# Kernel optimization log

Hardware: AMD Instinct MI355X
Metric: run time of the kernel (lower is better)

The kernel has to match this reference:

```python
import jax, jax.numpy as jnp
import numpy as np

N_NODES = 100000
N_EDGES = 3200000


def setup_inputs() -> dict:
    key = jax.random.key(0)
    ks = jax.random.split(key, 8)
    n_in, h1, h2 = 512, 512, 128
    # xavier-uniform-ish scaling for weights
    lim1 = (6.0 / (n_in + h1)) ** 0.5
    lim2 = (6.0 / (h1 + h2)) ** 0.5
    return {
        "seq_a": jax.random.normal(ks[0], (N_NODES, n_in), dtype=jnp.float32),
        "W1": jax.random.uniform(ks[1], (n_in, h1), jnp.float32, -lim1, lim1),
        "b1": jnp.zeros((h1,), jnp.float32),
        "W2": jax.random.uniform(ks[2], (h1, h2), jnp.float32, -lim2, lim2),
        "b2": jnp.zeros((h2,), jnp.float32),
        "adj_rows": jnp.sort(jax.random.randint(ks[3], (N_EDGES,), 0, N_NODES, jnp.int32)),
        "adj_cols": jax.random.randint(ks[4], (N_EDGES,), 0, N_NODES, jnp.int32),
        "adj_vals": jax.random.uniform(ks[5], (N_EDGES,), jnp.float32),
    }


def reference(seq_a, W1, b1, W2, b2, adj_rows, adj_cols, adj_vals):
    # Eval-mode forward: F.dropout is identity when training=False.
    # MLP: Linear(n_in,512) + ReLU, Linear(512,128) (no activation on last layer)
    h = jax.nn.relu(seq_a @ W1 + b1)          # [N, 512]
    h_a = h @ W2 + b2                          # [N, 128]
    # Sparse aggregation: h_p = adj @ h_a with adj in COO form.
    # h_p[r] = sum over edges e with row r of vals[e] * h_a[cols[e]]
    msgs = adj_vals[:, None] * h_a[adj_cols]   # [E, 128] irregular gather
    h_p = jax.ops.segment_sum(msgs, adj_rows, num_segments=N_NODES)  # [N, 128]
    return (h_a, h_p)
```

## Files before the change

kernel.cpp:

```cpp
#include <hip/hip_runtime.h>

#define N_NODES 100000
#define ROWS_PAD 100096
#define NIN 512
#define H1  512
#define H2  128
#define N_EDGES 3200000

typedef __attribute__((ext_vector_type(8))) short bf16x8;
typedef __attribute__((ext_vector_type(4))) float f32x4;
typedef __attribute__((ext_vector_type(2))) float f32x2;

__device__ __forceinline__ unsigned short f2b(float x) {
  union { float f; unsigned int u; } c; c.f = x;
  unsigned int u = c.u;
  unsigned int r = (u + 0x7FFFu + ((u >> 16) & 1u)) >> 16;
  return (unsigned short)r;
}

typedef const __attribute__((address_space(1))) unsigned int* gp1_t;
typedef __attribute__((address_space(3))) unsigned int* sp3_t;
__device__ __forceinline__ void gl_lds16(const void* g, void* s) {
  __builtin_amdgcn_global_load_lds((gp1_t)g, (sp3_t)s, 16, 0, 0);
}

__global__ void prep_a_kernel(const float* __restrict__ A, unsigned short* __restrict__ A1) {
  int idx = blockIdx.x * blockDim.x + threadIdx.x;
  int stride = gridDim.x * blockDim.x;
  for (int i = idx; i < N_NODES * 64; i += stride) {
    int n = i >> 6;
    int kb = (i & 63) << 3;
    int ks = kb ^ ((n & 7) << 3);
    const float* src = A + ((size_t)n << 9) + ks;
    float4 v0 = *(const float4*)src;
    float4 v1 = *(const float4*)(src + 4);
    uint4 p;
    p.x = (unsigned)f2b(v0.x) | ((unsigned)f2b(v0.y) << 16);
    p.y = (unsigned)f2b(v0.z) | ((unsigned)f2b(v0.w) << 16);
    p.z = (unsigned)f2b(v1.x) | ((unsigned)f2b(v1.y) << 16);
    p.w = (unsigned)f2b(v1.z) | ((unsigned)f2b(v1.w) << 16);
    *(uint4*)(A1 + ((size_t)n << 9) + kb) = p;
  }
}

__global__ void prep_w_kernel(const float* __restrict__ W1, const float* __restrict__ W2,
                              unsigned short* __restrict__ W1t, unsigned short* __restrict__ W2t) {
  int idx = blockIdx.x * blockDim.x + threadIdx.x;
  int stride = gridDim.x * blockDim.x;
  for (int i = idx; i < H1 * NIN; i += stride) {
    int n = i >> 9, k = i & 511;
    W1t[i] = f2b(W1[(size_t)(k ^ ((n & 7) << 3)) * H1 + n]);
  }
  for (int i = idx; i < H2 * H1; i += stride) {
    int n = i >> 9, k = i & 511;
    W2t[i] = f2b(W2[(size_t)(k ^ ((n & 7) << 3)) * H2 + n]);
  }
}

__global__ void rowptr_kernel(const int* __restrict__ rows, int* __restrict__ row_ptr) {
  int idx = blockIdx.x * blockDim.x + threadIdx.x;
  int stride = gridDim.x * blockDim.x;
  for (int e = idx; e < N_EDGES; e += stride) {
    int r = rows[e];
    int rp = (e == 0) ? -1 : rows[e - 1];
    for (int q = rp + 1; q <= r; ++q) row_ptr[q] = e;
  }
  int lastrow = rows[N_EDGES - 1];
  for (int q = idx; q <= N_NODES; q += stride)
    if (q > lastrow) row_ptr[q] = N_EDGES;
}

__global__ __launch_bounds__(256, 5) void gemm1_kernel(
    const unsigned short* __restrict__ A1, const unsigned short* __restrict__ W1t,
    const float* __restrict__ b1, unsigned short* __restrict__ h_pre)
{
  __shared__ __align__(16) unsigned short SM[12288];
  const int tid = threadIdx.x;
  const int w = tid >> 6, lane = tid & 63;
  const int l15 = lane & 15, lg = lane >> 4;
  const int wr = w & 1, wc = w >> 1;
  const int hw = blockIdx.x;
  const int work = (hw & 7) * 782 + (hw >> 3);
  const int row0 = (work >> 2) << 6;
  const int n0 = (work & 3) << 7;

  f32x4 acc[2][4];
  #pragma unroll
  for (int m = 0; m < 2; ++m)
    #pragma unroll
    for (int n = 0; n < 4; ++n) acc[m][n] = (f32x4){0.f, 0.f, 0.f, 0.f};

  const int so = tid * 16;
  for (int kt = 0; kt < 8; ++kt) {
    #pragma unroll
    for (int it = 0; it < 2; ++it) {
      int o = it * 4096 + so;
      int r = o >> 7, kb = o & 127;
      gl_lds16((const char*)A1 + (((size_t)(row0 + r)) << 10) + (kt << 7) + kb, (char*)SM + o);
    }
    #pragma unroll
    for (int it = 0; it < 4; ++it) {
      int o = it * 4096 + so;
      int r = o >> 7, kb = o & 127;
      gl_lds16((const char*)W1t + (((size_t)(n0 + r)) << 10) + (kt << 7) + kb, (char*)SM + 8192 + o);
    }
    __syncthreads();
    #pragma unroll
    for (int ks = 0; ks < 2; ++ks) {
      bf16x8 af[2], bfr[4];
      #pragma unroll
      for (int m = 0; m < 2; ++m) {
        int r = wr * 32 + m * 16 + l15;
        af[m] = *(const bf16x8*)((const char*)SM + (r << 7) + (((ks << 6) + (lg << 4)) ^ ((r & 7) << 4)));
      }
      #pragma unroll
      for (int n = 0; n < 4; ++n) {
        int r = wc * 64 + n * 16 + l15;
        bfr[n] = *(const bf16x8*)((const char*)SM + 8192 + (r << 7) + (((ks << 6) + (lg << 4)) ^ ((r & 7) << 4)));
      }
      #pragma unroll
      for (int m = 0; m < 2; ++m)
        #pragma unroll
        for (int n = 0; n < 4; ++n)
          acc[m][n] = __builtin_amdgcn_mfma_f32_16x16x32_bf16(af[m], bfr[n], acc[m][n], 0, 0, 0);
    }
    __syncthreads();
  }

  #pragma unroll
  for (int n = 0; n < 4; ++n) {
    int cl = wc * 64 + n * 16 + l15;
    float bias = b1[n0 + cl];
    #pragma unroll
    for (int m = 0; m < 2; ++m) {
      #pragma unroll
      for (int q = 0; q < 4; ++q) {
        int rl = wr * 32 + m * 16 + lg * 4 + q;
        float v = acc[m][n][q] + bias;
        v = v > 0.f ? v : 0.f;
        SM[rl * 128 + (cl ^ ((rl & 7) << 3))] = f2b(v);
      }
    }
  }
  __syncthreads();
  #pragma unroll
  for (int p = 0; p < 4; ++p) {
    int ch = tid + p * 256;
    int row = ch >> 4, six = ch & 15;
    uint4 d = *(const uint4*)((const char*)SM + (ch << 4));
    *(uint4*)((char*)h_pre + (((size_t)(row0 + row)) << 10) + (n0 << 1) + (six << 4)) = d;
  }
}

__global__ __launch_bounds__(256, 5) void gemm2_kernel(
    const unsigned short* __restrict__ Hp, const unsigned short* __restrict__ W2t,
    const float* __restrict__ b2, float* __restrict__ ha_out, unsigned char* __restrict__ ha8)
{
  __shared__ __align__(16) unsigned short SM[12288];
  const int tid = threadIdx.x;
  const int w = tid >> 6, lane = tid & 63;
  const int l15 = lane & 15, lg = lane >> 4;
  const int wr = w & 1, wc = w >> 1;
  const int row0 = blockIdx.x << 6;

  f32x4 acc[2][4];
  #pragma unroll
  for (int m = 0; m < 2; ++m)
    #pragma unroll
    for (int n = 0; n < 4; ++n) acc[m][n] = (f32x4){0.f, 0.f, 0.f, 0.f};

  const int so = tid * 16;
  for (int kt = 0; kt < 8; ++kt) {
    #pragma unroll
    for (int it = 0; it < 2; ++it) {
      int o = it * 4096 + so;
      int r = o >> 7, kb = o & 127;
      gl_lds16((const char*)Hp + (((size_t)(row0 + r)) << 10) + (kt << 7) + kb, (char*)SM + o);
    }
    #pragma unroll
    for (int it = 0; it < 4; ++it) {
      int o = it * 4096 + so;
      int r = o >> 7, kb = o & 127;
      gl_lds16((const char*)W2t + (((size_t)r) << 10) + (kt << 7) + kb, (char*)SM + 8192 + o);
    }
    __syncthreads();
    #pragma unroll
    for (int ks = 0; ks < 2; ++ks) {
      bf16x8 af[2], bfr[4];
      #pragma unroll
      for (int m = 0; m < 2; ++m) {
        int r = wr * 32 + m * 16 + l15;
        af[m] = *(const bf16x8*)((const char*)SM + (r << 7) + (((ks << 6) + (lg << 4)) ^ ((r & 7) << 4)));
      }
      #pragma unroll
      for (int n = 0; n < 4; ++n) {
        int r = wc * 64 + n * 16 + l15;
        bfr[n] = *(const bf16x8*)((const char*)SM + 8192 + (r << 7) + (((ks << 6) + (lg << 4)) ^ ((r & 7) << 4)));
      }
      #pragma unroll
      for (int m = 0; m < 2; ++m)
        #pragma unroll
        for (int n = 0; n < 4; ++n)
          acc[m][n] = __builtin_amdgcn_mfma_f32_16x16x32_bf16(af[m], bfr[n], acc[m][n], 0, 0, 0);
    }
    __syncthreads();
  }

  #pragma unroll
  for (int n = 0; n < 4; ++n) {
    int col = wc * 64 + n * 16 + l15;
    float bias = b2[col];
    #pragma unroll
    for (int m = 0; m < 2; ++m) {
      #pragma unroll
      for (int q = 0; q < 4; ++q) {
        int row = row0 + wr * 32 + m * 16 + lg * 4 + q;
        if (row < N_NODES) {
          float v = acc[m][n][q] + bias;
          ha_out[((size_t)row << 7) + col] = v;
          int p8 = __builtin_amdgcn_cvt_pk_fp8_f32(v, v, 0, false);
          ha8[((size_t)row << 7) + col] = (unsigned char)(p8 & 0xff);
        }
      }
    }
  }
}

__global__ __launch_bounds__(256) void agg_csr_kernel(
    const int* __restrict__ row_ptr, const int* __restrict__ cols, const float* __restrict__ vals,
    const unsigned char* __restrict__ gtab8, float* __restrict__ hp)
{
  const int row = __builtin_amdgcn_readfirstlane((blockIdx.x * blockDim.x + threadIdx.x) >> 6);
  if (row >= N_NODES) return;
  const int lane = threadIdx.x & 63;
  const int e0 = row_ptr[row];
  const int e1 = row_ptr[row + 1];

  float acc0 = 0.f, acc1 = 0.f;
  int e = e0;
  for (; e + 8 <= e1; e += 8) {
    int c[8]; float v[8]; unsigned short g[8];
    #pragma unroll
    for (int j = 0; j < 8; ++j) { c[j] = cols[e + j]; v[j] = vals[e + j]; }
    #pragma unroll
    for (int j = 0; j < 8; ++j)
      g[j] = *(const unsigned short*)(gtab8 + ((size_t)c[j] << 7) + (lane << 1));
    float t0 = acc0, t1 = 0.f, u0 = acc1, u1 = 0.f;
    #pragma unroll
    for (int j = 0; j < 8; j += 2) {
      f32x2 f0 = __builtin_amdgcn_cvt_pk_f32_fp8((int)g[j+0], false);
      f32x2 f1 = __builtin_amdgcn_cvt_pk_f32_fp8((int)g[j+1], false);
      t0 = fmaf(v[j+0], f0.x, t0);
      t1 = fmaf(v[j+1], f1.x, t1);
      u0 = fmaf(v[j+0], f0.y, u0);
      u1 = fmaf(v[j+1], f1.y, u1);
    }
    acc0 = t0 + t1; acc1 = u0 + u1;
  }
  for (; e < e1; ++e) {
    int c = cols[e];
    float v = vals[e];
    unsigned short g = *(const unsigned short*)(gtab8 + ((size_t)c << 7) + (lane << 1));
    f32x2 f = __builtin_amdgcn_cvt_pk_f32_fp8((int)g, false);
    acc0 = fmaf(v, f.x, acc0);
    acc1 = fmaf(v, f.y, acc1);
  }
  float2 st; st.x = acc0; st.y = acc1;
  *(float2*)&hp[((size_t)row << 7) + (lane << 1)] = st;
}

extern "C" void kernel_launch(void* const* d_in, const int* in_sizes, int n_in,
                              void* d_out, int out_size, void* d_ws, size_t ws_size,
                              hipStream_t stream) {
  const float* seq_a    = (const float*)d_in[0];
  const float* W1       = (const float*)d_in[1];
  const float* b1       = (const float*)d_in[2];
  const float* W2       = (const float*)d_in[3];
  const float* b2       = (const float*)d_in[4];
  const int*   adj_rows = (const int*)d_in[5];
  const int*   adj_cols = (const int*)d_in[6];
  const float* adj_vals = (const float*)d_in[7];

  unsigned short* A1    = (unsigned short*)d_ws;
  unsigned short* h_pre = A1 + (size_t)ROWS_PAD * NIN;
  unsigned short* W1t   = h_pre + (size_t)ROWS_PAD * H1;
  unsigned short* W2t   = W1t + (size_t)H1 * NIN;
  unsigned char*  ha8   = (unsigned char*)(W2t + (size_t)H2 * H1);
  int*            row_ptr = (int*)(ha8 + (size_t)N_NODES * H2);

  float* ha_out = (float*)d_out;
  float* hp     = ha_out + (size_t)N_NODES * H2;

  prep_a_kernel<<<2048, 256, 0, stream>>>(seq_a, A1);
  prep_w_kernel<<<1280, 256, 0, stream>>>(W1, W2, W1t, W2t);
  rowptr_kernel<<<2048, 256, 0, stream>>>(adj_rows, row_ptr);
  gemm1_kernel<<<6256, 256, 0, stream>>>(A1, W1t, b1, h_pre);
  gemm2_kernel<<<1564, 256, 0, stream>>>(h_pre, W2t, b2, ha_out, ha8);
  agg_csr_kernel<<<(ROWS_PAD * 64) / 256, 256, 0, stream>>>(row_ptr, adj_cols, adj_vals, ha8, hp);
}
```

Measured before the change: 301.7 us.

## Fuse fp32-to-bf16 conversion of input into GEMM1 tile loading

Removes the separate prep pass that converted seq_a to a swizzled bf16 copy. GEMM1 now loads fp32 rows directly into registers, packs them with v_cvt_pk_bf16_f32, and writes them into the swizzled LDS tile. This eliminates a full write and re-read of the bf16 activation buffer. In exchange, GEMM1 reads twice as many bytes per A tile, repeated across the column tiles, and the A path becomes register-staged instead of async global-to-LDS.

```diff
diff --git a/kernel.cpp b/kernel.cpp
--- a/kernel.cpp
+++ b/kernel.cpp
@@ -24,23 +24,10 @@
   __builtin_amdgcn_global_load_lds((gp1_t)g, (sp3_t)s, 16, 0, 0);
 }
 
-__global__ void prep_a_kernel(const float* __restrict__ A, unsigned short* __restrict__ A1) {
-  int idx = blockIdx.x * blockDim.x + threadIdx.x;
-  int stride = gridDim.x * blockDim.x;
-  for (int i = idx; i < N_NODES * 64; i += stride) {
-    int n = i >> 6;
-    int kb = (i & 63) << 3;
-    int ks = kb ^ ((n & 7) << 3);
-    const float* src = A + ((size_t)n << 9) + ks;
-    float4 v0 = *(const float4*)src;
-    float4 v1 = *(const float4*)(src + 4);
-    uint4 p;
-    p.x = (unsigned)f2b(v0.x) | ((unsigned)f2b(v0.y) << 16);
-    p.y = (unsigned)f2b(v0.z) | ((unsigned)f2b(v0.w) << 16);
-    p.z = (unsigned)f2b(v1.x) | ((unsigned)f2b(v1.y) << 16);
-    p.w = (unsigned)f2b(v1.z) | ((unsigned)f2b(v1.w) << 16);
-    *(uint4*)(A1 + ((size_t)n << 9) + kb) = p;
-  }
+__device__ __forceinline__ unsigned cvtpk(float lo, float hi) {
+  unsigned r;
+  asm("v_cvt_pk_bf16_f32 %0, %1, %2" : "=v"(r) : "v"(lo), "v"(hi));
+  return r;
 }
 
 __global__ void prep_w_kernel(const float* __restrict__ W1, const float* __restrict__ W2,
@@ -71,7 +58,7 @@
 }
 
 __global__ __launch_bounds__(256, 5) void gemm1_kernel(
-    const unsigned short* __restrict__ A1, const unsigned short* __restrict__ W1t,
+    const float* __restrict__ A, const unsigned short* __restrict__ W1t,
     const float* __restrict__ b1, unsigned short* __restrict__ h_pre)
 {
   __shared__ __align__(16) unsigned short SM[12288];
@@ -84,6 +71,14 @@
   const int row0 = (work >> 2) << 6;
   const int n0 = (work & 3) << 7;
 
+  int arow = row0 + (tid >> 2);
+  if (arow > N_NODES - 1) arow = N_NODES - 1;
+  const float* asrc = A + ((size_t)arow << 9) + ((tid & 3) << 4);
+  const int alr  = tid >> 2;
+  const int aswz = (alr & 7) << 4;
+  const int ad0  = ((tid & 3) << 5);
+  char* alds = (char*)SM + alr * 128;
+
   f32x4 acc[2][4];
   #pragma unroll
   for (int m = 0; m < 2; ++m)
@@ -92,18 +87,24 @@
 
   const int so = tid * 16;
   for (int kt = 0; kt < 8; ++kt) {
-    #pragma unroll
-    for (int it = 0; it < 2; ++it) {
-      int o = it * 4096 + so;
-      int r = o >> 7, kb = o & 127;
-      gl_lds16((const char*)A1 + (((size_t)(row0 + r)) << 10) + (kt << 7) + kb, (char*)SM + o);
-    }
+    const float* ap = asrc + (kt << 6);
+    f32x4 a0 = *(const f32x4*)(ap);
+    f32x4 a1 = *(const f32x4*)(ap + 4);
+    f32x4 a2 = *(const f32x4*)(ap + 8);
+    f32x4 a3 = *(const f32x4*)(ap + 12);
     #pragma unroll
     for (int it = 0; it < 4; ++it) {
       int o = it * 4096 + so;
       int r = o >> 7, kb = o & 127;
       gl_lds16((const char*)W1t + (((size_t)(n0 + r)) << 10) + (kt << 7) + kb, (char*)SM + 8192 + o);
     }
+    uint4 w0, w1;
+    w0.x = cvtpk(a0[0], a0[1]); w0.y = cvtpk(a0[2], a0[3]);
+    w0.z = cvtpk(a1[0], a1[1]); w0.w = cvtpk(a1[2], a1[3]);
+    w1.x = cvtpk(a2[0], a2[1]); w1.y = cvtpk(a2[2], a2[3]);
+    w1.z = cvtpk(a3[0], a3[1]); w1.w = cvtpk(a3[2], a3[3]);
+    *(uint4*)(alds + ((ad0 +  0) ^ aswz)) = w0;
+    *(uint4*)(alds + ((ad0 + 16) ^ aswz)) = w1;
     __syncthreads();
     #pragma unroll
     for (int ks = 0; ks < 2; ++ks) {
@@ -281,8 +282,7 @@
   const int*   adj_cols = (const int*)d_in[6];
   const float* adj_vals = (const float*)d_in[7];
 
-  unsigned short* A1    = (unsigned short*)d_ws;
-  unsigned short* h_pre = A1 + (size_t)ROWS_PAD * NIN;
+  unsigned short* h_pre = (unsigned short*)d_ws;
   unsigned short* W1t   = h_pre + (size_t)ROWS_PAD * H1;
   unsigned short* W2t   = W1t + (size_t)H1 * NIN;
   unsigned char*  ha8   = (unsigned char*)(W2t + (size_t)H2 * H1);
@@ -291,10 +291,9 @@
   float* ha_out = (float*)d_out;
   float* hp     = ha_out + (size_t)N_NODES * H2;
 
-  prep_a_kernel<<<2048, 256, 0, stream>>>(seq_a, A1);
   prep_w_kernel<<<1280, 256, 0, stream>>>(W1, W2, W1t, W2t);
   rowptr_kernel<<<2048, 256, 0, stream>>>(adj_rows, row_ptr);
-  gemm1_kernel<<<6256, 256, 0, stream>>>(A1, W1t, b1, h_pre);
+  gemm1_kernel<<<6256, 256, 0, stream>>>(seq_a, W1t, b1, h_pre);
   gemm2_kernel<<<1564, 256, 0, stream>>>(h_pre, W2t, b2, ha_out, ha8);
   agg_csr_kernel<<<(ROWS_PAD * 64) / 256, 256, 0, stream>>>(row_ptr, adj_cols, adj_vals, ha8, hp);
 }
```

Result: faster. 287.4 us (-4.7%).
